# Kernel tuning notes

Measured on AMD Instinct MI355X. Metric: run time of the kernel, lower is better.

The kernel has to match this reference:

```python
import jax, jax.numpy as jnp
import numpy as np

NOISE_RATIO = 25
NORM_TERM = 9.0

def setup_inputs() -> dict:
    key = jax.random.key(0)
    k1, k2, k3, k4, k5 = jax.random.split(key, 5)
    N, E, V, K = 4096, 1024, 50257, NOISE_RATIO
    x = jax.random.normal(k1, (N, E), dtype=jnp.float32)
    target = jax.random.randint(k2, (N,), 0, V)
    noise_idx = jax.random.randint(k3, (N, K), 0, V)
    # decoder params per IndexLinear.reset_parameters: weight ~ U(-0.1, 0.1), bias = 0
    weight = jax.random.uniform(k4, (V, E), dtype=jnp.float32, minval=-0.1, maxval=0.1)
    bias = jnp.zeros((V,), dtype=jnp.float32)
    # noise distribution over the vocab (positive, normalized)
    noise = jax.random.uniform(k5, (V,), dtype=jnp.float32, minval=0.1, maxval=1.0)
    noise = noise / jnp.sum(noise)
    return {"x": x, "target": target, "noise_idx": noise_idx,
            "weight": weight, "bias": bias, "noise": noise}

def reference(x, target, noise_idx, weight, bias, noise):
    """NCE loss (training branch), size_average=True.
    x: (N, E), target: (N,), noise_idx: (N, K), weight: (V, E), bias: (V,), noise: (V,)
    """
    N = x.shape[0]
    k = jnp.float32(NOISE_RATIO)
    # IndexLinear: gather rows for [target | noise] then per-sample (1,E)@(E,1+K)
    idx = jnp.concatenate([target[:, None], noise_idx], axis=1)   # (N, 1+K)
    w_rows = weight[idx]                                          # (N, 1+K, E)
    b_rows = bias[idx]                                            # (N, 1+K)
    logits = b_rows + jnp.einsum('ne,nke->nk', x, w_rows)         # (N, 1+K)
    probs = jnp.exp(logits - NORM_TERM)
    data_prob = probs[:, 0]                                       # (N,)
    noise_in_data = probs[:, 1:]                                  # (N, K)
    pn_target = noise[target]                                     # (N,)
    pn_noise = noise[noise_idx]                                   # (N, K)
    rnn_loss = jnp.log(data_prob / (data_prob + k * pn_target))
    noise_loss = jnp.sum(jnp.log(k * pn_noise / (noise_in_data + k * pn_noise)), axis=1)
    loss = -jnp.sum(rnn_loss + noise_loss)
    return loss / N
```

## Files before the change

kernel.cpp:

```cpp
#include <hip/hip_runtime.h>
#include <hip/hip_bf16.h>


#define NN 4096
#define EE 1024
#define KK 25

__global__ __launch_bounds__(256) void nce_block_kernel(
    const float* __restrict__ x,
    const int* __restrict__ target,
    const int* __restrict__ noise_idx,
    const float* __restrict__ weight,
    const float* __restrict__ bias,
    const float* __restrict__ noise,
    float* __restrict__ block_loss)
{
    const int n = blockIdx.x;
    __shared__ float xs[EE];
    __shared__ float logits[32];

    const float4* x4 = (const float4*)(x + (size_t)n * EE);
    float4* xs4 = (float4*)xs;
    xs4[threadIdx.x] = x4[threadIdx.x];
    __syncthreads();

    const int wave = threadIdx.x >> 6;
    const int lane = threadIdx.x & 63;

    for (int j = wave; j < KK + 1; j += 4) {
        const int row = (j == 0) ? target[n] : noise_idx[n * KK + (j - 1)];
        const float4* w4 = (const float4*)(weight + (size_t)row * EE);
        float acc = 0.0f;
#pragma unroll
        for (int p = 0; p < 4; ++p) {
            float4 xv = xs4[p * 64 + lane];
            float4 wv = w4[p * 64 + lane];
            acc += xv.x * wv.x + xv.y * wv.y + xv.z * wv.z + xv.w * wv.w;
        }
#pragma unroll
        for (int off = 32; off > 0; off >>= 1)
            acc += __shfl_down(acc, off);
        if (lane == 0) logits[j] = acc + bias[row];
    }
    __syncthreads();

    if (threadIdx.x == 0) {
        const float kf = (float)KK;
        float p0 = expf(logits[0] - 9.0f);
        float pt = noise[target[n]];
        float loss = logf(p0 / (p0 + kf * pt));
#pragma unroll 5
        for (int j = 1; j <= KK; ++j) {
            float pj = expf(logits[j] - 9.0f);
            float pn25 = kf * noise[noise_idx[n * KK + (j - 1)]];
            loss += logf(pn25 / (pj + pn25));
        }
        block_loss[n] = -loss;
    }
}

__global__ __launch_bounds__(256) void nce_reduce_kernel(
    const float* __restrict__ block_loss, float* __restrict__ out)
{
    float acc = 0.0f;
    for (int i = threadIdx.x; i < NN; i += 256)
        acc += block_loss[i];
#pragma unroll
    for (int off = 32; off > 0; off >>= 1)
        acc += __shfl_down(acc, off);
    __shared__ float s[4];
    const int wave = threadIdx.x >> 6;
    const int lane = threadIdx.x & 63;
    if (lane == 0) s[wave] = acc;
    __syncthreads();
    if (threadIdx.x == 0)
        out[0] = (s[0] + s[1] + s[2] + s[3]) / (float)NN;
}

extern "C" void kernel_launch(void* const* d_in, const int* in_sizes, int n_in,
                              void* d_out, int out_size, void* d_ws, size_t ws_size,
                              hipStream_t stream) {
    const float* x        = (const float*)d_in[0];
    const int*   target   = (const int*)d_in[1];
    const int*   noiseIdx = (const int*)d_in[2];
    const float* weight   = (const float*)d_in[3];
    const float* bias     = (const float*)d_in[4];
    const float* noise    = (const float*)d_in[5];
    float* out = (float*)d_out;
    float* block_loss = (float*)d_ws;

    nce_block_kernel<<<NN, 256, 0, stream>>>(x, target, noiseIdx, weight, bias, noise, block_loss);
    nce_reduce_kernel<<<1, 256, 0, stream>>>(block_loss, out);
}
```

Before: 321.4 us.

## Keep x in registers, batch gathered row loads, distribute loss math across waves

Each wave now holds its slice of the x row in registers instead of staging it through shared memory, which removes one barrier. The per-row loop is fully unrolled into up to seven independent weight-row gathers, so more global loads are in flight at once. The per-row exp/log loss terms are computed by each wave's lane 0 instead of serially by a single thread. The cost is higher register pressure from the unrolled loads, which may lower occupancy.

```diff
diff --git a/kernel.cpp b/kernel.cpp
--- a/kernel.cpp
+++ b/kernel.cpp
@@ -6,7 +6,11 @@
 #define EE 1024
 #define KK 25
 
-__global__ __launch_bounds__(256) void nce_block_kernel(
+__device__ __forceinline__ void fma4(float4& a, const float4& p, const float4& q) {
+    a.x += p.x * q.x; a.y += p.y * q.y; a.z += p.z * q.z; a.w += p.w * q.w;
+}
+
+__global__ __launch_bounds__(256) void nce_main_kernel(
     const float* __restrict__ x,
     const int* __restrict__ target,
     const int* __restrict__ noise_idx,
@@ -16,47 +20,69 @@
     float* __restrict__ block_loss)
 {
     const int n = blockIdx.x;
-    __shared__ float xs[EE];
-    __shared__ float logits[32];
-
-    const float4* x4 = (const float4*)(x + (size_t)n * EE);
-    float4* xs4 = (float4*)xs;
-    xs4[threadIdx.x] = x4[threadIdx.x];
-    __syncthreads();
-
     const int wave = threadIdx.x >> 6;
     const int lane = threadIdx.x & 63;
 
-    for (int j = wave; j < KK + 1; j += 4) {
-        const int row = (j == 0) ? target[n] : noise_idx[n * KK + (j - 1)];
-        const float4* w4 = (const float4*)(weight + (size_t)row * EE);
-        float acc = 0.0f;
+    const float4* x4 = (const float4*)(x + (size_t)n * EE);
+    const float4 xr0 = x4[lane];
+    const float4 xr1 = x4[64 + lane];
+    const float4 xr2 = x4[128 + lane];
+    const float4 xr3 = x4[192 + lane];
+
+    const int nj = (wave < 2) ? 7 : 6;
+
+    float sacc[7];
+    int rows[7];
+
 #pragma unroll
-        for (int p = 0; p < 4; ++p) {
-            float4 xv = xs4[p * 64 + lane];
-            float4 wv = w4[p * 64 + lane];
-            acc += xv.x * wv.x + xv.y * wv.y + xv.z * wv.z + xv.w * wv.w;
+    for (int jj = 0; jj < 7; ++jj) {
+        const int j = wave + (jj << 2);
+        const bool valid = (jj < nj);
+        int row = 0;
+        float4 a = make_float4(0.f, 0.f, 0.f, 0.f);
+        if (valid) {
+            row = (j == 0) ? target[n] : noise_idx[n * KK + (j - 1)];
+            const float4* w4 = (const float4*)(weight + (size_t)row * EE);
+            const float4 w0 = w4[lane];
+            const float4 w1 = w4[64 + lane];
+            const float4 w2 = w4[128 + lane];
+            const float4 w3 = w4[192 + lane];
+            fma4(a, xr0, w0);
+            fma4(a, xr1, w1);
+            fma4(a, xr2, w2);
+            fma4(a, xr3, w3);
         }
+        rows[jj] = row;
+        sacc[jj] = (a.x + a.y) + (a.z + a.w);
+    }
+
+#pragma unroll
+    for (int jj = 0; jj < 7; ++jj) {
 #pragma unroll
         for (int off = 32; off > 0; off >>= 1)
-            acc += __shfl_down(acc, off);
-        if (lane == 0) logits[j] = acc + bias[row];
+            sacc[jj] += __shfl_xor(sacc[jj], off);
+    }
+
+    __shared__ float swave[4];
+    if (lane == 0) {
+        float part = 0.0f;
+#pragma unroll
+        for (int jj = 0; jj < 7; ++jj) {
+            if (jj < nj) {
+                const int j = wave + (jj << 2);
+                const int row = rows[jj];
+                const float logit = sacc[jj] + bias[row];
+                const float p = expf(logit - 9.0f);
+                const float pn25 = 25.0f * noise[row];
+                part += (j == 0) ? logf(p / (p + pn25))
+                                 : logf(pn25 / (p + pn25));
+            }
+        }
+        swave[wave] = part;
     }
     __syncthreads();
-
-    if (threadIdx.x == 0) {
-        const float kf = (float)KK;
-        float p0 = expf(logits[0] - 9.0f);
-        float pt = noise[target[n]];
-        float loss = logf(p0 / (p0 + kf * pt));
-#pragma unroll 5
-        for (int j = 1; j <= KK; ++j) {
-            float pj = expf(logits[j] - 9.0f);
-            float pn25 = kf * noise[noise_idx[n * KK + (j - 1)]];
-            loss += logf(pn25 / (pj + pn25));
-        }
-        block_loss[n] = -loss;
-    }
+    if (threadIdx.x == 0)
+        block_loss[n] = -((swave[0] + swave[1]) + (swave[2] + swave[3]));
 }
 
 __global__ __launch_bounds__(256) void nce_reduce_kernel(
@@ -74,7 +100,7 @@
     if (lane == 0) s[wave] = acc;
     __syncthreads();
     if (threadIdx.x == 0)
-        out[0] = (s[0] + s[1] + s[2] + s[3]) / (float)NN;
+        out[0] = ((s[0] + s[1]) + (s[2] + s[3])) / (float)NN;
 }
 
 extern "C" void kernel_launch(void* const* d_in, const int* in_sizes, int n_in,
@@ -89,6 +115,6 @@
     float* out = (float*)d_out;
     float* block_loss = (float*)d_ws;
 
-    nce_block_kernel<<<NN, 256, 0, stream>>>(x, target, noiseIdx, weight, bias, noise, block_loss);
+    nce_main_kernel<<<NN, 256, 0, stream>>>(x, target, noiseIdx, weight, bias, noise, block_loss);
     nce_reduce_kernel<<<1, 256, 0, stream>>>(block_loss, out);
 }
```

After: 315.4 us. Within noise of the previous version (-1.9%).
